# Performance work log

Measured on AMD Instinct MI355X. Metric: run time of the kernel, lower is better.

## Reference

```python
import jax, jax.numpy as jnp
import numpy as np
from jax import lax

K = 3
STRIDE = 2
PADDING = 1
OUTPUT_PADDING = 1


def setup_inputs() -> dict:
    key = jax.random.key(0)
    k1, k2, k3, k4 = jax.random.split(key, 4)
    B, C, H, W = 4, 64, 128, 128
    outC = 64
    g_ch = 3
    x = jax.random.normal(k1, (B, C, H, W), dtype=jnp.float32)
    guide = jax.random.normal(k2, (B, g_ch, H * STRIDE, W * STRIDE), dtype=jnp.float32)
    # kaiming-uniform-like init scale: bound = 1/sqrt(fan_in), fan_in = C*K*K
    fan_in = C * K * K
    bound = 1.0 / np.sqrt(fan_in)
    weight = jax.random.uniform(k3, (C, outC, K, K), dtype=jnp.float32, minval=-bound, maxval=bound)
    bias = jax.random.uniform(k4, (outC,), dtype=jnp.float32, minval=-bound, maxval=bound)
    return {"x": x, "guide": guide, "weight": weight, "bias": bias}


def _patches(t, pad):
    # torch.nn.functional.unfold equivalent: channel ordering (C, kh, kw)
    return lax.conv_general_dilated_patches(
        t, filter_shape=(K, K), window_strides=(1, 1), padding=[(pad, pad), (pad, pad)]
    )


def reference(x, guide, weight, bias):
    B, C, H, W = x.shape
    _, g_ch, GH, GW = guide.shape
    s, p, op = STRIDE, PADDING, OUTPUT_PADDING

    # Gaussian affinity kernel from guide patches
    gp = (K - 1) // 2
    guide_unf = _patches(guide, gp).reshape(B, g_ch, K * K, GH, GW)
    diff = guide_unf - guide_unf[:, :, K * K // 2 : K * K // 2 + 1]
    kern = jnp.exp(-0.5 * jnp.sum(diff * diff, axis=1))  # [B, K*K, GH, GW]
    kern = kern.reshape(B, 1, K, K, GH, GW)

    # depthwise transposed conv with all-ones 1x1 kernel == zero-stuffing upsample
    Ht, Wt = (H - 1) * s + 1, (W - 1) * s + 1
    temp = jnp.zeros((B, C, Ht, Wt), dtype=x.dtype).at[:, :, ::s, ::s].set(x)
    pad = (K - 1) - p
    temp = jnp.pad(temp, ((0, 0), (0, 0), (pad, pad + op), (pad, pad + op)))

    cols = _patches(temp, 0).reshape(B, C, K, K, GH, GW)
    in_mul_k = cols * kern  # [B, C, K, K, GH, GW]
    out = jnp.einsum("bcklhw,cokl->bohw", in_mul_k, weight)
    return out + bias.reshape(1, -1, 1, 1)
```

## Files before the change

### kernel.cpp

```cpp
#include <hip/hip_runtime.h>
#include <math.h>

typedef __attribute__((ext_vector_type(8))) short short8;
typedef __attribute__((ext_vector_type(4))) float float4v;
typedef __attribute__((ext_vector_type(4))) unsigned int uint4v;

#define GH_ 256
#define GW_ 256
#define H_  128
#define W_  128
#define C_  64
#define OC_ 64
#define NB_ 4

static __device__ __forceinline__ unsigned short f2bf(float f) {
    union { float f; unsigned int u; } v; v.f = f;
    unsigned int u = v.u;
    unsigned int r = u + 0x7FFFu + ((u >> 16) & 1u);
    return (unsigned short)(r >> 16);
}

static __device__ __forceinline__ int swz(int byte) {
    return byte ^ (((byte >> 7) & 7) << 4);
}

__global__ __launch_bounds__(512) void prep_w(const float* __restrict__ w,
                                              unsigned short* __restrict__ wtb) {
    const int t = blockIdx.x;
    const int kh = t / 3, kw = t - kh * 3;
    for (int i = threadIdx.x; i < OC_ * C_; i += 512) {
        int c = i & 63, o = (i >> 6) & 63;
        wtb[t * OC_ * C_ + i] = f2bf(w[((c * OC_ + o) * 3 + kh) * 3 + kw]);
    }
}

__global__ __launch_bounds__(1024, 4) void pac_fused(
    const float* __restrict__ x,
    const float* __restrict__ guide,
    const unsigned short* __restrict__ wtb,
    const float* __restrict__ bias,
    float* __restrict__ out)
{
    __shared__ unsigned short xt[3 * 128 * 64];
    __shared__ float klds[9][2][128];

    const int ypair = blockIdx.x;
    const int b     = blockIdx.y;
    const int tid   = threadIdx.x;
    const int R0    = ypair * 2;

    {
        const int col = tid & 127;
        const int cg  = tid >> 7;
        #pragma unroll
        for (int lr = 0; lr < 3; ++lr) {
            int srow = R0 + lr; if (srow > H_ - 1) srow = H_ - 1;
            const float* xs = x + (((size_t)(b * C_ + cg * 8) * H_) + srow) * W_ + col;
            float v[8];
            #pragma unroll
            for (int j = 0; j < 8; ++j) v[j] = xs[(size_t)j * H_ * W_];
            unsigned int p0 = (unsigned int)f2bf(v[0]) | ((unsigned int)f2bf(v[1]) << 16);
            unsigned int p1 = (unsigned int)f2bf(v[2]) | ((unsigned int)f2bf(v[3]) << 16);
            unsigned int p2 = (unsigned int)f2bf(v[4]) | ((unsigned int)f2bf(v[5]) << 16);
            unsigned int p3 = (unsigned int)f2bf(v[6]) | ((unsigned int)f2bf(v[7]) << 16);
            int byte = ((lr * 128 + col) << 7) + cg * 16;
            *(uint4v*)((char*)xt + swz(byte)) = (uint4v){p0, p1, p2, p3};
        }
    }

    for (int i = tid; i < 9 * 256; i += 1024) {
        int px = i & 255, gs = i >> 8;
        int py = px >> 7, xp = px & 127;
        int lhp = (gs < 3) ? 0 : 1;
        int ls  = (gs < 3) ? gs : gs - 3;
        int lntr = 1 + lhp;
        int wp, r, q;
        if (ls < lntr) { wp = 0; r = ls; q = 0; }
        else { int s = ls - lntr; wp = 1; r = s >> 1; q = s & 1; }
        int yp = R0 + py;
        int h = 2 * yp + lhp, w = 2 * xp + wp;
        int rr = yp + r, cl = xp + q;
        float kv = 0.f;
        if (rr < H_ && cl < W_) {
            int hh = rr * 2, ww = cl * 2;
            const float* gb = guide + (size_t)b * 3 * GH_ * GW_;
            float s2 = 0.f;
            #pragma unroll
            for (int g = 0; g < 3; ++g) {
                float d = gb[(g * GH_ + hh) * GW_ + ww] - gb[(g * GH_ + h) * GW_ + w];
                s2 += d * d;
            }
            kv = __expf(-0.5f * s2);
        }
        klds[gs][py][xp] = kv;
    }
    __syncthreads();

    const int wave = tid >> 6, lane = tid & 63;
    const int l16 = lane & 15, qk = lane >> 4;
    const int oh  = wave & 1;
    const int py  = (wave >> 1) & 1;
    const int xh  = (wave >> 2) & 1;
    const int hp  = wave >> 3;
    const int obase = oh * 32;
    const int xpb   = xh * 64;
    const int yp = R0 + py;
    const int h  = 2 * yp + hp;
    const int ntr = 1 + hp;
    const int kbase = hp ? 3 : 0;

    for (int mf = 0; mf < 2; ++mf) {
        float acc0[4][4];
        float acc1[4][4];
        #pragma unroll
        for (int nf = 0; nf < 4; ++nf)
            #pragma unroll
            for (int e = 0; e < 4; ++e) { acc0[nf][e] = 0.f; acc1[nf][e] = 0.f; }

        const int o = obase + mf * 16 + l16;

        for (int r = 0; r <= hp; ++r) {
            int kh = hp ? 2 * r : 1;
            int rowc = yp + r; if (rowc > H_ - 1) rowc = H_ - 1;
            int lr0 = rowc - R0;
            int s_c = kbase + r;
            int s_l = kbase + ntr + 2 * r;
            int s_r = kbase + ntr + 2 * r + 1;

            short8 af[3][2];
            #pragma unroll
            for (int kw3 = 0; kw3 < 3; ++kw3) {
                const short8* wbase = (const short8*)(wtb + (size_t)(kh * 3 + kw3) * OC_ * C_);
                af[kw3][0] = wbase[(o * C_ + qk * 8) >> 3];
                af[kw3][1] = wbase[(o * C_ + 32 + qk * 8) >> 3];
            }

            #pragma unroll
            for (int nf = 0; nf < 4; ++nf) {
                int xp = xpb + nf * 16 + l16;
                int col1 = xp + 1; if (col1 > W_ - 1) col1 = W_ - 1;
                int base0 = ((lr0 * 128 + xp)   << 7) + qk * 16;
                int base1 = ((lr0 * 128 + col1) << 7) + qk * 16;
                short8 b0a = *(const short8*)((const char*)xt + swz(base0));
                short8 b0b = *(const short8*)((const char*)xt + swz(base0 + 64));
                short8 b1a = *(const short8*)((const char*)xt + swz(base1));
                short8 b1b = *(const short8*)((const char*)xt + swz(base1 + 64));
                float kc = klds[s_c][py][xp];
                float kl = klds[s_l][py][xp];
                float kr = klds[s_r][py][xp];
                float4v d;
                d = (float4v){0.f, 0.f, 0.f, 0.f};
                d = __builtin_amdgcn_mfma_f32_16x16x32_bf16(af[1][0], b0a, d, 0, 0, 0);
                d = __builtin_amdgcn_mfma_f32_16x16x32_bf16(af[1][1], b0b, d, 0, 0, 0);
                #pragma unroll
                for (int e = 0; e < 4; ++e) acc0[nf][e] += kc * d[e];
                d = (float4v){0.f, 0.f, 0.f, 0.f};
                d = __builtin_amdgcn_mfma_f32_16x16x32_bf16(af[0][0], b0a, d, 0, 0, 0);
                d = __builtin_amdgcn_mfma_f32_16x16x32_bf16(af[0][1], b0b, d, 0, 0, 0);
                #pragma unroll
                for (int e = 0; e < 4; ++e) acc1[nf][e] += kl * d[e];
                d = (float4v){0.f, 0.f, 0.f, 0.f};
                d = __builtin_amdgcn_mfma_f32_16x16x32_bf16(af[2][0], b1a, d, 0, 0, 0);
                d = __builtin_amdgcn_mfma_f32_16x16x32_bf16(af[2][1], b1b, d, 0, 0, 0);
                #pragma unroll
                for (int e = 0; e < 4; ++e) acc1[nf][e] += kr * d[e];
            }
        }

        float bv[4];
        #pragma unroll
        for (int e = 0; e < 4; ++e)
            bv[e] = bias[obase + mf * 16 + qk * 4 + e];

        #pragma unroll
        for (int e = 0; e < 4; ++e) {
            int oo = obase + mf * 16 + qk * 4 + e;
            float2* op = (float2*)(out + (((size_t)b * OC_ + oo) * GH_ + h) * GW_);
            #pragma unroll
            for (int nf = 0; nf < 4; ++nf) {
                int xp = xpb + nf * 16 + l16;
                float2 v;
                v.x = acc0[nf][e] + bv[e];
                v.y = acc1[nf][e] + bv[e];
                op[xp] = v;
            }
        }
    }
}

extern "C" void kernel_launch(void* const* d_in, const int* in_sizes, int n_in,
                              void* d_out, int out_size, void* d_ws, size_t ws_size,
                              hipStream_t stream) {
    const float* x     = (const float*)d_in[0];
    const float* guide = (const float*)d_in[1];
    const float* wgt   = (const float*)d_in[2];
    const float* bias  = (const float*)d_in[3];
    float* out = (float*)d_out;

    unsigned short* wtb = (unsigned short*)d_ws;

    prep_w<<<dim3(9), 512, 0, stream>>>(wgt, wtb);
    pac_fused<<<dim3(64, 4), 1024, 0, stream>>>(x, guide, wtb, bias, out);
}
```

Before: 103.4 us.

## Fuse weight prep into main kernel via atomic ticket and flag wait

Drops the separate weight-conversion kernel. The first nine blocks to take an atomic ticket each convert one kernel tap of the weights to bf16. All blocks then spin on a completion counter before running the MFMA stage. The aim is to remove one kernel launch and the serialization between the two kernels, overlapping weight prep with the x/guide staging. In exchange it adds a memset, atomics, a grid-wide spin wait that assumes co-residency of the ticket holders, and a cross-block visibility risk if the cache scopes are not handled correctly.

```diff
diff --git a/kernel.cpp b/kernel.cpp
--- a/kernel.cpp
+++ b/kernel.cpp
@@ -24,30 +24,41 @@
     return byte ^ (((byte >> 7) & 7) << 4);
 }
 
-__global__ __launch_bounds__(512) void prep_w(const float* __restrict__ w,
-                                              unsigned short* __restrict__ wtb) {
-    const int t = blockIdx.x;
-    const int kh = t / 3, kw = t - kh * 3;
-    for (int i = threadIdx.x; i < OC_ * C_; i += 512) {
-        int c = i & 63, o = (i >> 6) & 63;
-        wtb[t * OC_ * C_ + i] = f2bf(w[((c * OC_ + o) * 3 + kh) * 3 + kw]);
-    }
-}
-
 __global__ __launch_bounds__(1024, 4) void pac_fused(
     const float* __restrict__ x,
     const float* __restrict__ guide,
-    const unsigned short* __restrict__ wtb,
+    const float* __restrict__ wgt,
     const float* __restrict__ bias,
+    unsigned short* __restrict__ wtb,
+    unsigned int* __restrict__ flags,
     float* __restrict__ out)
 {
     __shared__ unsigned short xt[3 * 128 * 64];
     __shared__ float klds[9][2][128];
+    __shared__ unsigned int sticket;
 
     const int ypair = blockIdx.x;
     const int b     = blockIdx.y;
     const int tid   = threadIdx.x;
     const int R0    = ypair * 2;
+
+    if (tid == 0)
+        sticket = __hip_atomic_fetch_add(&flags[0], 1u, __ATOMIC_RELAXED,
+                                         __HIP_MEMORY_SCOPE_AGENT);
+    __syncthreads();
+    if (sticket < 9u) {
+        const int t = (int)sticket;
+        for (int i = tid; i < OC_ * C_; i += 1024) {
+            int c = i & 63, o = (i >> 6) & 63;
+            wtb[t * OC_ * C_ + i] = f2bf(wgt[(c * OC_ + o) * 9 + t]);
+        }
+        __syncthreads();
+        if (tid == 0) {
+            __threadfence();
+            __hip_atomic_fetch_add(&flags[1], 1u, __ATOMIC_RELEASE,
+                                   __HIP_MEMORY_SCOPE_AGENT);
+        }
+    }
 
     {
         const int col = tid & 127;
@@ -93,6 +104,13 @@
             kv = __expf(-0.5f * s2);
         }
         klds[gs][py][xp] = kv;
+    }
+    __syncthreads();
+
+    if (tid == 0) {
+        while (__hip_atomic_load(&flags[1], __ATOMIC_ACQUIRE,
+                                 __HIP_MEMORY_SCOPE_AGENT) < 9u)
+            __builtin_amdgcn_s_sleep(8);
     }
     __syncthreads();
 
@@ -198,7 +216,8 @@
     float* out = (float*)d_out;
 
     unsigned short* wtb = (unsigned short*)d_ws;
-
-    prep_w<<<dim3(9), 512, 0, stream>>>(wgt, wtb);
-    pac_fused<<<dim3(64, 4), 1024, 0, stream>>>(x, guide, wtb, bias, out);
-}
+    unsigned int* flags = (unsigned int*)((char*)d_ws + 9 * OC_ * C_ * sizeof(unsigned short));
+
+    hipMemsetAsync(flags, 0, 16, stream);
+    pac_fused<<<dim3(64, 4), 1024, 0, stream>>>(x, guide, wgt, bias, wtb, flags, out);
+}
```

Result: slower. 109.1 us (+5.5%).
